# Optimization experiments

Measured on AMD Instinct MI355X. Metric: run time of the kernel, lower is better.

The kernel has to match this reference:

```python
import jax, jax.numpy as jnp
import numpy as np

X_SIZE, Y_SIZE, C_SIZE, H = 4, 2, 3, 128
B, C_CTX, T = 4, 512, 512


def _xavier(key, shape):
    fan_in, fan_out = shape[0], shape[1]
    a = jnp.sqrt(6.0 / (fan_in + fan_out))
    return jax.random.uniform(key, shape, jnp.float32, -a, a)


def setup_inputs() -> dict:
    key = jax.random.key(0)
    ks = jax.random.split(key, 9)
    return {
        "context_x": jax.random.normal(ks[0], (B, C_CTX, X_SIZE), jnp.float32),
        "context_y": jax.random.normal(ks[1], (B, C_CTX, Y_SIZE), jnp.float32),
        "target_x": jax.random.normal(ks[2], (B, T, X_SIZE), jnp.float32),
        "W_in": _xavier(ks[3], (C_SIZE + Y_SIZE, H)),
        "b_in": jnp.zeros((H,), jnp.float32),
        "W_ctx": _xavier(ks[4], (C_SIZE, H)),
        "b_ctx": jnp.zeros((H,), jnp.float32),
        "W_tgt": _xavier(ks[5], (H, H)),
        "b_tgt": jnp.zeros((H,), jnp.float32),
    }


def reference(context_x, context_y, target_x, W_in, b_in, W_ctx, b_ctx, W_tgt, b_tgt):
    ctx_c = context_x[..., :C_SIZE]                         # [B, C, c]
    # value: projected concat of context coords + context values
    enc_in = jnp.concatenate([ctx_c, context_y], axis=-1)   # [B, C, c+y]
    value = enc_in @ W_in + b_in                            # [B, C, H]
    key_ = ctx_c @ W_ctx + b_ctx                            # [B, C, H]
    query = target_x[..., :C_SIZE] @ W_ctx + b_ctx          # [B, T, H]
    # L1-distance attention scores: -sum_h |0.5*(key - query)|
    diff = (key_[:, None, :, :] - query[:, :, None, :]) * 0.5  # [B, T, C, H]
    scores = -jnp.sum(jnp.abs(diff), axis=-1)               # [B, T, C]
    w = jax.nn.softmax(scores, axis=-1)                     # [B, T, C]
    rep = jnp.einsum('btc,bch->bth', w, value)              # [B, T, H]
    return rep @ W_tgt + b_tgt
```

## Files before the change

kernel.cpp:

```cpp
#include <hip/hip_runtime.h>

#define BB 4
#define CC 512
#define TDIM 512
#define HH 128
#define TT 8
#define NR 4
#define CPW 128

__global__ __launch_bounds__(128) void prep_kernel(
    const float* __restrict__ ctx_x, const float* __restrict__ ctx_y,
    const float* __restrict__ tgt_x,
    const float* __restrict__ W_in, const float* __restrict__ b_in,
    const float* __restrict__ W_ctx, const float* __restrict__ b_ctx,
    float* __restrict__ key, float* __restrict__ query, float* __restrict__ value)
{
    int row = blockIdx.x;
    int h   = threadIdx.x;

    float4 cx = ((const float4*)ctx_x)[row];
    float2 cy = ((const float2*)ctx_y)[row];
    float4 tx = ((const float4*)tgt_x)[row];

    float wi0 = W_in[0*HH+h], wi1 = W_in[1*HH+h], wi2 = W_in[2*HH+h];
    float wi3 = W_in[3*HH+h], wi4 = W_in[4*HH+h];
    float wc0 = W_ctx[0*HH+h], wc1 = W_ctx[1*HH+h], wc2 = W_ctx[2*HH+h];
    float bi  = b_in[h], bc = b_ctx[h];

    value[row*HH+h] = fmaf(cx.x,wi0, fmaf(cx.y,wi1, fmaf(cx.z,wi2, fmaf(cy.x,wi3, fmaf(cy.y,wi4, bi)))));
    key  [row*HH+h] = fmaf(cx.x,wc0, fmaf(cx.y,wc1, fmaf(cx.z,wc2, bc)));
    query[row*HH+h] = fmaf(tx.x,wc0, fmaf(tx.y,wc1, fmaf(tx.z,wc2, bc)));
}

__global__ __launch_bounds__(512) void fused_kernel(
    const float* __restrict__ key, const float* __restrict__ query,
    const float* __restrict__ value, const float* __restrict__ W_tgt,
    const float* __restrict__ b_tgt, float* __restrict__ out)
{
    const int bx   = blockIdx.x;
    const int b    = bx >> 6;
    const int t0   = (bx & 63) * TT;
    const int tid  = threadIdx.x;
    const int wave = tid >> 6;
    const int cr   = wave & 3;
    const int th   = wave >> 2;
    const int lane = tid & 63;

    __shared__ __align__(16) float sbuf[8][4][128];
    __shared__ __align__(16) float pTbuf[8][128][4];
    __shared__ __align__(16) float2 ml[8][4];

    float (*rep)[HH]        = (float (*)[HH])&sbuf[0][0][0];
    float (*partial)[4][HH] = (float (*)[4][HH])&pTbuf[0][0][0];

    const int cl = lane >> 3;
    const int hq = lane & 7;
    float4 qr[4][4];
    #pragma unroll
    for (int tt = 0; tt < 4; ++tt)
        #pragma unroll
        for (int j = 0; j < 4; ++j)
            qr[tt][j] = *(const float4*)&query[(b*TDIM + t0 + th*4 + tt)*HH + j*32 + hq*4];

    #pragma unroll 1
    for (int pp = 0; pp < 4; ++pp) {
        const int crow = cr*CPW + pp*32 + cl*4;
        const float* kp = &key[(b*CC + crow)*HH];
        float a0[4], a1[4], a2[4], a3[4];
        #pragma unroll
        for (int tt = 0; tt < 4; ++tt) { a0[tt]=0.f; a1[tt]=0.f; a2[tt]=0.f; a3[tt]=0.f; }
        #pragma unroll
        for (int j = 0; j < 4; ++j) {
            const int hb = j*32 + hq*4;
            float4 k0 = *(const float4*)(kp + 0*HH + hb);
            float4 k1 = *(const float4*)(kp + 1*HH + hb);
            float4 k2 = *(const float4*)(kp + 2*HH + hb);
            float4 k3 = *(const float4*)(kp + 3*HH + hb);
            #pragma unroll
            for (int tt = 0; tt < 4; ++tt) {
                float4 qv = qr[tt][j];
                a0[tt] += fabsf(k0.x-qv.x)+fabsf(k0.y-qv.y)+fabsf(k0.z-qv.z)+fabsf(k0.w-qv.w);
                a1[tt] += fabsf(k1.x-qv.x)+fabsf(k1.y-qv.y)+fabsf(k1.z-qv.z)+fabsf(k1.w-qv.w);
                a2[tt] += fabsf(k2.x-qv.x)+fabsf(k2.y-qv.y)+fabsf(k2.z-qv.z)+fabsf(k2.w-qv.w);
                a3[tt] += fabsf(k3.x-qv.x)+fabsf(k3.y-qv.y)+fabsf(k3.z-qv.z)+fabsf(k3.w-qv.w);
            }
        }
        #pragma unroll
        for (int tt = 0; tt < 4; ++tt) {
            float v0=a0[tt], v1=a1[tt], v2=a2[tt], v3=a3[tt];
            v0 += __shfl_xor(v0,1); v0 += __shfl_xor(v0,2); v0 += __shfl_xor(v0,4);
            v1 += __shfl_xor(v1,1); v1 += __shfl_xor(v1,2); v1 += __shfl_xor(v1,4);
            v2 += __shfl_xor(v2,1); v2 += __shfl_xor(v2,2); v2 += __shfl_xor(v2,4);
            v3 += __shfl_xor(v3,1); v3 += __shfl_xor(v3,2); v3 += __shfl_xor(v3,4);
            if (hq == 0)
                *(float4*)&sbuf[wave][tt][pp*32 + cl*4] =
                    make_float4(-0.5f*v0, -0.5f*v1, -0.5f*v2, -0.5f*v3);
        }
    }

    {
        const int tg = lane >> 4, ci = lane & 15;
        float4 x0 = *(const float4*)&sbuf[wave][tg][ci*8];
        float4 x1 = *(const float4*)&sbuf[wave][tg][ci*8 + 4];
        float m = fmaxf(fmaxf(fmaxf(x0.x,x0.y), fmaxf(x0.z,x0.w)),
                        fmaxf(fmaxf(x1.x,x1.y), fmaxf(x1.z,x1.w)));
        m = fmaxf(m, __shfl_xor(m,1)); m = fmaxf(m, __shfl_xor(m,2));
        m = fmaxf(m, __shfl_xor(m,4)); m = fmaxf(m, __shfl_xor(m,8));
        float e0 = __expf(x0.x-m), e1 = __expf(x0.y-m), e2 = __expf(x0.z-m), e3 = __expf(x0.w-m);
        float e4 = __expf(x1.x-m), e5 = __expf(x1.y-m), e6 = __expf(x1.z-m), e7 = __expf(x1.w-m);
        float sm = ((e0+e1)+(e2+e3)) + ((e4+e5)+(e6+e7));
        sm += __shfl_xor(sm,1); sm += __shfl_xor(sm,2);
        sm += __shfl_xor(sm,4); sm += __shfl_xor(sm,8);
        pTbuf[wave][ci*8+0][tg] = e0;  pTbuf[wave][ci*8+1][tg] = e1;
        pTbuf[wave][ci*8+2][tg] = e2;  pTbuf[wave][ci*8+3][tg] = e3;
        pTbuf[wave][ci*8+4][tg] = e4;  pTbuf[wave][ci*8+5][tg] = e5;
        pTbuf[wave][ci*8+6][tg] = e6;  pTbuf[wave][ci*8+7][tg] = e7;
        if (ci == 0) ml[wave][tg] = make_float2(m, sm);
    }

    const int cs = lane >> 5, hv = lane & 31;
    {
        float4 acc[4];
        #pragma unroll
        for (int tt = 0; tt < 4; ++tt) acc[tt] = make_float4(0.f,0.f,0.f,0.f);
        const float* vp = &value[(b*CC + cr*CPW + cs*64)*HH + hv*4];
        #pragma unroll 4
        for (int i = 0; i < 64; ++i) {
            float4 p4 = *(const float4*)&pTbuf[wave][cs*64 + i][0];
            float4 vv = *(const float4*)(vp + i*HH);
            acc[0].x=fmaf(p4.x,vv.x,acc[0].x); acc[0].y=fmaf(p4.x,vv.y,acc[0].y);
            acc[0].z=fmaf(p4.x,vv.z,acc[0].z); acc[0].w=fmaf(p4.x,vv.w,acc[0].w);
            acc[1].x=fmaf(p4.y,vv.x,acc[1].x); acc[1].y=fmaf(p4.y,vv.y,acc[1].y);
            acc[1].z=fmaf(p4.y,vv.z,acc[1].z); acc[1].w=fmaf(p4.y,vv.w,acc[1].w);
            acc[2].x=fmaf(p4.z,vv.x,acc[2].x); acc[2].y=fmaf(p4.z,vv.y,acc[2].y);
            acc[2].z=fmaf(p4.z,vv.z,acc[2].z); acc[2].w=fmaf(p4.z,vv.w,acc[2].w);
            acc[3].x=fmaf(p4.w,vv.x,acc[3].x); acc[3].y=fmaf(p4.w,vv.y,acc[3].y);
            acc[3].z=fmaf(p4.w,vv.z,acc[3].z); acc[3].w=fmaf(p4.w,vv.w,acc[3].w);
        }
        #pragma unroll
        for (int tt = 0; tt < 4; ++tt) {
            acc[tt].x += __shfl_xor(acc[tt].x, 32);
            acc[tt].y += __shfl_xor(acc[tt].y, 32);
            acc[tt].z += __shfl_xor(acc[tt].z, 32);
            acc[tt].w += __shfl_xor(acc[tt].w, 32);
        }
        if (cs == 0) {
            #pragma unroll
            for (int tt = 0; tt < 4; ++tt)
                *(float4*)&partial[wave][tt][hv*4] = acc[tt];
        }
    }
    __syncthreads();

    #pragma unroll
    for (int e = tid; e < TT*HH; e += 512) {
        const int t = e >> 7, h = e & 127;
        const int thh = t >> 2, tt = t & 3;
        float2 q0 = ml[thh*4+0][tt], q1 = ml[thh*4+1][tt];
        float2 q2 = ml[thh*4+2][tt], q3 = ml[thh*4+3][tt];
        float M = fmaxf(fmaxf(q0.x,q1.x), fmaxf(q2.x,q3.x));
        float a0 = __expf(q0.x-M), a1 = __expf(q1.x-M);
        float a2 = __expf(q2.x-M), a3 = __expf(q3.x-M);
        float L = fmaf(a0,q0.y, fmaf(a1,q1.y, fmaf(a2,q2.y, a3*q3.y)));
        float r = a0*partial[thh*4+0][tt][h] + a1*partial[thh*4+1][tt][h]
                + a2*partial[thh*4+2][tt][h] + a3*partial[thh*4+3][tt][h];
        rep[t][h] = r / L;
    }
    __syncthreads();

    {
        const int lt = tid >> 7, h = tid & 127;
        float o0 = b_tgt[h], o1 = o0;
        for (int k = 0; k < HH; k += 4) {
            float4 r0 = *(const float4*)&rep[lt    ][k];
            float4 r1 = *(const float4*)&rep[lt + 4][k];
            float w0 = W_tgt[(k+0)*HH + h];
            float w1 = W_tgt[(k+1)*HH + h];
            float w2 = W_tgt[(k+2)*HH + h];
            float w3 = W_tgt[(k+3)*HH + h];
            o0 = fmaf(r0.x,w0, fmaf(r0.y,w1, fmaf(r0.z,w2, fmaf(r0.w,w3, o0))));
            o1 = fmaf(r1.x,w0, fmaf(r1.y,w1, fmaf(r1.z,w2, fmaf(r1.w,w3, o1))));
        }
        out[(b*TDIM + t0 + lt    )*HH + h] = o0;
        out[(b*TDIM + t0 + lt + 4)*HH + h] = o1;
    }
}

extern "C" void kernel_launch(void* const* d_in, const int* in_sizes, int n_in,
                              void* d_out, int out_size, void* d_ws, size_t ws_size,
                              hipStream_t stream) {
    const float* ctx_x = (const float*)d_in[0];
    const float* ctx_y = (const float*)d_in[1];
    const float* tgt_x = (const float*)d_in[2];
    const float* W_in  = (const float*)d_in[3];
    const float* b_in  = (const float*)d_in[4];
    const float* W_ctx = (const float*)d_in[5];
    const float* b_ctx = (const float*)d_in[6];
    const float* W_tgt = (const float*)d_in[7];
    const float* b_tgt = (const float*)d_in[8];

    float* ws    = (float*)d_ws;
    float* key   = ws;
    float* query = ws + 1*BB*CC*HH;
    float* value = ws + 2*BB*CC*HH;

    prep_kernel<<<BB*CC, 128, 0, stream>>>(ctx_x, ctx_y, tgt_x,
                                           W_in, b_in, W_ctx, b_ctx,
                                           key, query, value);
    fused_kernel<<<BB*(TDIM/TT), 512, 0, stream>>>(key, query, value,
                                                   W_tgt, b_tgt, (float*)d_out);
}
```

Before: 32.49 us.

## Split fused attention into context-split score/PV kernel plus separate projection kernel

Replaces the single fused kernel (256 blocks of 512 threads, 8 targets each) with a score+PV kernel over 1024 blocks of 256 threads, each handling 4 targets and half of the context. Partial softmax numerators and (max, sum) statistics go to workspace, and a new projection kernel merges the two halves and applies W_tgt. The goal is more blocks for better occupancy and load balance across the GPU. The cost is an extra kernel launch and a global-memory round trip for the partial results.

```diff
diff --git a/kernel.cpp b/kernel.cpp
--- a/kernel.cpp
+++ b/kernel.cpp
@@ -4,9 +4,6 @@
 #define CC 512
 #define TDIM 512
 #define HH 128
-#define TT 8
-#define NR 4
-#define CPW 128
 
 __global__ __launch_bounds__(128) void prep_kernel(
     const float* __restrict__ ctx_x, const float* __restrict__ ctx_y,
@@ -32,43 +29,43 @@
     query[row*HH+h] = fmaf(tx.x,wc0, fmaf(tx.y,wc1, fmaf(tx.z,wc2, bc)));
 }
 
-__global__ __launch_bounds__(512) void fused_kernel(
+__global__ __launch_bounds__(256) void score_pv_kernel(
     const float* __restrict__ key, const float* __restrict__ query,
-    const float* __restrict__ value, const float* __restrict__ W_tgt,
-    const float* __restrict__ b_tgt, float* __restrict__ out)
+    const float* __restrict__ value,
+    float* __restrict__ bp, float2* __restrict__ bml)
 {
-    const int bx   = blockIdx.x;
-    const int b    = bx >> 6;
-    const int t0   = (bx & 63) * TT;
-    const int tid  = threadIdx.x;
-    const int wave = tid >> 6;
-    const int cr   = wave & 3;
-    const int th   = wave >> 2;
-    const int lane = tid & 63;
-
-    __shared__ __align__(16) float sbuf[8][4][128];
-    __shared__ __align__(16) float pTbuf[8][128][4];
-    __shared__ __align__(16) float2 ml[8][4];
-
-    float (*rep)[HH]        = (float (*)[HH])&sbuf[0][0][0];
-    float (*partial)[4][HH] = (float (*)[4][HH])&pTbuf[0][0][0];
+    const int bx    = blockIdx.x;
+    const int chalf = bx & 1;
+    const int tq    = (bx >> 1) & 127;
+    const int b     = bx >> 8;
+    const int t0    = tq * 4;
+    const int c0    = chalf * 256;
+    const int tid   = threadIdx.x;
+    const int w     = tid >> 6;
+    const int lane  = tid & 63;
+
+    __shared__ __align__(16) float s_w[4][4][64];
+    __shared__ __align__(16) float pT_w[4][64][4];
+    __shared__ __align__(16) float2 wml[4][4];
+    __shared__ __align__(16) float partial[4][4][HH];
 
     const int cl = lane >> 3;
     const int hq = lane & 7;
     float4 qr[4][4];
     #pragma unroll
-    for (int tt = 0; tt < 4; ++tt)
+    for (int t = 0; t < 4; ++t)
         #pragma unroll
         for (int j = 0; j < 4; ++j)
-            qr[tt][j] = *(const float4*)&query[(b*TDIM + t0 + th*4 + tt)*HH + j*32 + hq*4];
+            qr[t][j] = *(const float4*)&query[(b*TDIM + t0 + t)*HH + j*32 + hq*4];
+
+    const int cw0 = c0 + w*64;
 
     #pragma unroll 1
-    for (int pp = 0; pp < 4; ++pp) {
-        const int crow = cr*CPW + pp*32 + cl*4;
-        const float* kp = &key[(b*CC + crow)*HH];
+    for (int pass = 0; pass < 2; ++pass) {
+        const float* kp = &key[(b*CC + cw0 + pass*32 + cl*4)*HH];
         float a0[4], a1[4], a2[4], a3[4];
         #pragma unroll
-        for (int tt = 0; tt < 4; ++tt) { a0[tt]=0.f; a1[tt]=0.f; a2[tt]=0.f; a3[tt]=0.f; }
+        for (int t = 0; t < 4; ++t) { a0[t]=0.f; a1[t]=0.f; a2[t]=0.f; a3[t]=0.f; }
         #pragma unroll
         for (int j = 0; j < 4; ++j) {
             const int hb = j*32 + hq*4;
@@ -77,56 +74,54 @@
             float4 k2 = *(const float4*)(kp + 2*HH + hb);
             float4 k3 = *(const float4*)(kp + 3*HH + hb);
             #pragma unroll
-            for (int tt = 0; tt < 4; ++tt) {
-                float4 qv = qr[tt][j];
-                a0[tt] += fabsf(k0.x-qv.x)+fabsf(k0.y-qv.y)+fabsf(k0.z-qv.z)+fabsf(k0.w-qv.w);
-                a1[tt] += fabsf(k1.x-qv.x)+fabsf(k1.y-qv.y)+fabsf(k1.z-qv.z)+fabsf(k1.w-qv.w);
-                a2[tt] += fabsf(k2.x-qv.x)+fabsf(k2.y-qv.y)+fabsf(k2.z-qv.z)+fabsf(k2.w-qv.w);
-                a3[tt] += fabsf(k3.x-qv.x)+fabsf(k3.y-qv.y)+fabsf(k3.z-qv.z)+fabsf(k3.w-qv.w);
+            for (int t = 0; t < 4; ++t) {
+                float4 qv = qr[t][j];
+                a0[t] += fabsf(k0.x-qv.x)+fabsf(k0.y-qv.y)+fabsf(k0.z-qv.z)+fabsf(k0.w-qv.w);
+                a1[t] += fabsf(k1.x-qv.x)+fabsf(k1.y-qv.y)+fabsf(k1.z-qv.z)+fabsf(k1.w-qv.w);
+                a2[t] += fabsf(k2.x-qv.x)+fabsf(k2.y-qv.y)+fabsf(k2.z-qv.z)+fabsf(k2.w-qv.w);
+                a3[t] += fabsf(k3.x-qv.x)+fabsf(k3.y-qv.y)+fabsf(k3.z-qv.z)+fabsf(k3.w-qv.w);
             }
         }
         #pragma unroll
-        for (int tt = 0; tt < 4; ++tt) {
-            float v0=a0[tt], v1=a1[tt], v2=a2[tt], v3=a3[tt];
+        for (int t = 0; t < 4; ++t) {
+            float v0=a0[t], v1=a1[t], v2=a2[t], v3=a3[t];
             v0 += __shfl_xor(v0,1); v0 += __shfl_xor(v0,2); v0 += __shfl_xor(v0,4);
             v1 += __shfl_xor(v1,1); v1 += __shfl_xor(v1,2); v1 += __shfl_xor(v1,4);
             v2 += __shfl_xor(v2,1); v2 += __shfl_xor(v2,2); v2 += __shfl_xor(v2,4);
             v3 += __shfl_xor(v3,1); v3 += __shfl_xor(v3,2); v3 += __shfl_xor(v3,4);
             if (hq == 0)
-                *(float4*)&sbuf[wave][tt][pp*32 + cl*4] =
+                *(float4*)&s_w[w][t][pass*32 + cl*4] =
                     make_float4(-0.5f*v0, -0.5f*v1, -0.5f*v2, -0.5f*v3);
         }
     }
 
     {
         const int tg = lane >> 4, ci = lane & 15;
-        float4 x0 = *(const float4*)&sbuf[wave][tg][ci*8];
-        float4 x1 = *(const float4*)&sbuf[wave][tg][ci*8 + 4];
-        float m = fmaxf(fmaxf(fmaxf(x0.x,x0.y), fmaxf(x0.z,x0.w)),
-                        fmaxf(fmaxf(x1.x,x1.y), fmaxf(x1.z,x1.w)));
+        float4 x = *(const float4*)&s_w[w][tg][ci*4];
+        float m = fmaxf(fmaxf(x.x, x.y), fmaxf(x.z, x.w));
         m = fmaxf(m, __shfl_xor(m,1)); m = fmaxf(m, __shfl_xor(m,2));
         m = fmaxf(m, __shfl_xor(m,4)); m = fmaxf(m, __shfl_xor(m,8));
-        float e0 = __expf(x0.x-m), e1 = __expf(x0.y-m), e2 = __expf(x0.z-m), e3 = __expf(x0.w-m);
-        float e4 = __expf(x1.x-m), e5 = __expf(x1.y-m), e6 = __expf(x1.z-m), e7 = __expf(x1.w-m);
-        float sm = ((e0+e1)+(e2+e3)) + ((e4+e5)+(e6+e7));
+        float e0 = __expf(x.x-m), e1 = __expf(x.y-m);
+        float e2 = __expf(x.z-m), e3 = __expf(x.w-m);
+        float sm = (e0+e1) + (e2+e3);
         sm += __shfl_xor(sm,1); sm += __shfl_xor(sm,2);
         sm += __shfl_xor(sm,4); sm += __shfl_xor(sm,8);
-        pTbuf[wave][ci*8+0][tg] = e0;  pTbuf[wave][ci*8+1][tg] = e1;
-        pTbuf[wave][ci*8+2][tg] = e2;  pTbuf[wave][ci*8+3][tg] = e3;
-        pTbuf[wave][ci*8+4][tg] = e4;  pTbuf[wave][ci*8+5][tg] = e5;
-        pTbuf[wave][ci*8+6][tg] = e6;  pTbuf[wave][ci*8+7][tg] = e7;
-        if (ci == 0) ml[wave][tg] = make_float2(m, sm);
-    }
-
-    const int cs = lane >> 5, hv = lane & 31;
+        pT_w[w][ci*4+0][tg] = e0;
+        pT_w[w][ci*4+1][tg] = e1;
+        pT_w[w][ci*4+2][tg] = e2;
+        pT_w[w][ci*4+3][tg] = e3;
+        if (ci == 0) wml[w][tg] = make_float2(m, sm);
+    }
+
     {
+        const int cs = lane >> 5, hv = lane & 31;
         float4 acc[4];
         #pragma unroll
-        for (int tt = 0; tt < 4; ++tt) acc[tt] = make_float4(0.f,0.f,0.f,0.f);
-        const float* vp = &value[(b*CC + cr*CPW + cs*64)*HH + hv*4];
-        #pragma unroll 4
-        for (int i = 0; i < 64; ++i) {
-            float4 p4 = *(const float4*)&pTbuf[wave][cs*64 + i][0];
+        for (int t = 0; t < 4; ++t) acc[t] = make_float4(0.f,0.f,0.f,0.f);
+        const float* vp = &value[(b*CC + cw0 + cs*32)*HH + hv*4];
+        #pragma unroll 8
+        for (int i = 0; i < 32; ++i) {
+            float4 p4 = *(const float4*)&pT_w[w][cs*32 + i][0];
             float4 vv = *(const float4*)(vp + i*HH);
             acc[0].x=fmaf(p4.x,vv.x,acc[0].x); acc[0].y=fmaf(p4.x,vv.y,acc[0].y);
             acc[0].z=fmaf(p4.x,vv.z,acc[0].z); acc[0].w=fmaf(p4.x,vv.w,acc[0].w);
@@ -138,33 +133,58 @@
             acc[3].z=fmaf(p4.w,vv.z,acc[3].z); acc[3].w=fmaf(p4.w,vv.w,acc[3].w);
         }
         #pragma unroll
-        for (int tt = 0; tt < 4; ++tt) {
-            acc[tt].x += __shfl_xor(acc[tt].x, 32);
-            acc[tt].y += __shfl_xor(acc[tt].y, 32);
-            acc[tt].z += __shfl_xor(acc[tt].z, 32);
-            acc[tt].w += __shfl_xor(acc[tt].w, 32);
+        for (int t = 0; t < 4; ++t) {
+            acc[t].x += __shfl_xor(acc[t].x, 32);
+            acc[t].y += __shfl_xor(acc[t].y, 32);
+            acc[t].z += __shfl_xor(acc[t].z, 32);
+            acc[t].w += __shfl_xor(acc[t].w, 32);
         }
         if (cs == 0) {
             #pragma unroll
-            for (int tt = 0; tt < 4; ++tt)
-                *(float4*)&partial[wave][tt][hv*4] = acc[tt];
+            for (int t = 0; t < 4; ++t)
+                *(float4*)&partial[w][t][hv*4] = acc[t];
         }
     }
     __syncthreads();
 
     #pragma unroll
-    for (int e = tid; e < TT*HH; e += 512) {
+    for (int e = tid; e < 4*HH; e += 256) {
         const int t = e >> 7, h = e & 127;
-        const int thh = t >> 2, tt = t & 3;
-        float2 q0 = ml[thh*4+0][tt], q1 = ml[thh*4+1][tt];
-        float2 q2 = ml[thh*4+2][tt], q3 = ml[thh*4+3][tt];
+        float2 q0 = wml[0][t], q1 = wml[1][t], q2 = wml[2][t], q3 = wml[3][t];
         float M = fmaxf(fmaxf(q0.x,q1.x), fmaxf(q2.x,q3.x));
         float a0 = __expf(q0.x-M), a1 = __expf(q1.x-M);
         float a2 = __expf(q2.x-M), a3 = __expf(q3.x-M);
-        float L = fmaf(a0,q0.y, fmaf(a1,q1.y, fmaf(a2,q2.y, a3*q3.y)));
-        float r = a0*partial[thh*4+0][tt][h] + a1*partial[thh*4+1][tt][h]
-                + a2*partial[thh*4+2][tt][h] + a3*partial[thh*4+3][tt][h];
-        rep[t][h] = r / L;
+        float r = a0*partial[0][t][h] + a1*partial[1][t][h]
+                + a2*partial[2][t][h] + a3*partial[3][t][h];
+        bp[bx*512 + e] = r;
+        if (h == 0) {
+            float L = fmaf(a0,q0.y, fmaf(a1,q1.y, fmaf(a2,q2.y, a3*q3.y)));
+            bml[bx*4 + t] = make_float2(M, L);
+        }
+    }
+}
+
+__global__ __launch_bounds__(256) void proj_kernel(
+    const float* __restrict__ bp, const float2* __restrict__ bml,
+    const float* __restrict__ W_tgt, const float* __restrict__ b_tgt,
+    float* __restrict__ out)
+{
+    const int bx  = blockIdx.x;
+    const int b   = bx >> 7;
+    const int t0  = (bx & 127) * 4;
+    const int tid = threadIdx.x;
+    const int blk0 = bx*2, blk1 = bx*2 + 1;
+
+    __shared__ __align__(16) float rep[4][HH];
+
+    #pragma unroll
+    for (int e = tid; e < 4*HH; e += 256) {
+        const int t = e >> 7;
+        float2 m0 = bml[blk0*4 + t], m1 = bml[blk1*4 + t];
+        float M  = fmaxf(m0.x, m1.x);
+        float a0 = __expf(m0.x - M), a1 = __expf(m1.x - M);
+        float invL = 1.f / fmaf(a0, m0.y, a1 * m1.y);
+        (&rep[0][0])[e] = (a0*bp[blk0*512 + e] + a1*bp[blk1*512 + e]) * invL;
     }
     __syncthreads();
 
@@ -173,7 +193,7 @@
         float o0 = b_tgt[h], o1 = o0;
         for (int k = 0; k < HH; k += 4) {
             float4 r0 = *(const float4*)&rep[lt    ][k];
-            float4 r1 = *(const float4*)&rep[lt + 4][k];
+            float4 r1 = *(const float4*)&rep[lt + 2][k];
             float w0 = W_tgt[(k+0)*HH + h];
             float w1 = W_tgt[(k+1)*HH + h];
             float w2 = W_tgt[(k+2)*HH + h];
@@ -182,7 +202,7 @@
             o1 = fmaf(r1.x,w0, fmaf(r1.y,w1, fmaf(r1.z,w2, fmaf(r1.w,w3, o1))));
         }
         out[(b*TDIM + t0 + lt    )*HH + h] = o0;
-        out[(b*TDIM + t0 + lt + 4)*HH + h] = o1;
+        out[(b*TDIM + t0 + lt + 2)*HH + h] = o1;
     }
 }
 
@@ -203,10 +223,12 @@
     float* key   = ws;
     float* query = ws + 1*BB*CC*HH;
     float* value = ws + 2*BB*CC*HH;
+    float* bp    = ws + 3*BB*CC*HH;
+    float2* bml  = (float2*)(bp + 1024*512);
 
     prep_kernel<<<BB*CC, 128, 0, stream>>>(ctx_x, ctx_y, tgt_x,
                                            W_in, b_in, W_ctx, b_ctx,
                                            key, query, value);
-    fused_kernel<<<BB*(TDIM/TT), 512, 0, stream>>>(key, query, value,
-                                                   W_tgt, b_tgt, (float*)d_out);
-}
+    score_pv_kernel<<<BB*128*2, 256, 0, stream>>>(key, query, value, bp, bml);
+    proj_kernel<<<BB*128, 256, 0, stream>>>(bp, bml, W_tgt, b_tgt, (float*)d_out);
+}
```

Result: slower. 38.55 us (+18.6%).

## Split context across eight waves per target group using 1024-thread blocks

Applied to the files above, without the earlier changes.

Doubles the block to 1024 threads so each group of four targets is handled by eight waves, each covering 64 context rows instead of 128. Partial softmax statistics and weighted sums are merged across eight waves in the combine step, and each thread then produces one output row. This roughly halves the serial per-wave work, adding latency hiding within the only 256 blocks. The cost is more shared memory, a wider merge and register pressure at 1024-thread launch bounds, which could limit occupancy.

```diff
diff --git a/kernel.cpp b/kernel.cpp
--- a/kernel.cpp
+++ b/kernel.cpp
@@ -5,8 +5,6 @@
 #define TDIM 512
 #define HH 128
 #define TT 8
-#define NR 4
-#define CPW 128
 
 __global__ __launch_bounds__(128) void prep_kernel(
     const float* __restrict__ ctx_x, const float* __restrict__ ctx_y,
@@ -32,7 +30,7 @@
     query[row*HH+h] = fmaf(tx.x,wc0, fmaf(tx.y,wc1, fmaf(tx.z,wc2, bc)));
 }
 
-__global__ __launch_bounds__(512) void fused_kernel(
+__global__ __launch_bounds__(1024) void fused_kernel(
     const float* __restrict__ key, const float* __restrict__ query,
     const float* __restrict__ value, const float* __restrict__ W_tgt,
     const float* __restrict__ b_tgt, float* __restrict__ out)
@@ -42,16 +40,15 @@
     const int t0   = (bx & 63) * TT;
     const int tid  = threadIdx.x;
     const int wave = tid >> 6;
-    const int cr   = wave & 3;
-    const int th   = wave >> 2;
+    const int th   = wave >> 3;
+    const int cw   = wave & 7;
     const int lane = tid & 63;
 
-    __shared__ __align__(16) float sbuf[8][4][128];
-    __shared__ __align__(16) float pTbuf[8][128][4];
-    __shared__ __align__(16) float2 ml[8][4];
-
-    float (*rep)[HH]        = (float (*)[HH])&sbuf[0][0][0];
-    float (*partial)[4][HH] = (float (*)[4][HH])&pTbuf[0][0][0];
+    __shared__ __align__(16) float s_w[16][4][64];
+    __shared__ __align__(16) float pT_w[16][64][4];
+    __shared__ __align__(16) float2 wml[16][4];
+    __shared__ __align__(16) float partial[16][4][HH];
+    __shared__ __align__(16) float rep[TT][HH];
 
     const int cl = lane >> 3;
     const int hq = lane & 7;
@@ -62,10 +59,11 @@
         for (int j = 0; j < 4; ++j)
             qr[tt][j] = *(const float4*)&query[(b*TDIM + t0 + th*4 + tt)*HH + j*32 + hq*4];
 
+    const int cw0 = cw * 64;
+
     #pragma unroll 1
-    for (int pp = 0; pp < 4; ++pp) {
-        const int crow = cr*CPW + pp*32 + cl*4;
-        const float* kp = &key[(b*CC + crow)*HH];
+    for (int pass = 0; pass < 2; ++pass) {
+        const float* kp = &key[(b*CC + cw0 + pass*32 + cl*4)*HH];
         float a0[4], a1[4], a2[4], a3[4];
         #pragma unroll
         for (int tt = 0; tt < 4; ++tt) { a0[tt]=0.f; a1[tt]=0.f; a2[tt]=0.f; a3[tt]=0.f; }
@@ -93,40 +91,38 @@
             v2 += __shfl_xor(v2,1); v2 += __shfl_xor(v2,2); v2 += __shfl_xor(v2,4);
             v3 += __shfl_xor(v3,1); v3 += __shfl_xor(v3,2); v3 += __shfl_xor(v3,4);
             if (hq == 0)
-                *(float4*)&sbuf[wave][tt][pp*32 + cl*4] =
+                *(float4*)&s_w[wave][tt][pass*32 + cl*4] =
                     make_float4(-0.5f*v0, -0.5f*v1, -0.5f*v2, -0.5f*v3);
         }
     }
 
     {
         const int tg = lane >> 4, ci = lane & 15;
-        float4 x0 = *(const float4*)&sbuf[wave][tg][ci*8];
-        float4 x1 = *(const float4*)&sbuf[wave][tg][ci*8 + 4];
-        float m = fmaxf(fmaxf(fmaxf(x0.x,x0.y), fmaxf(x0.z,x0.w)),
-                        fmaxf(fmaxf(x1.x,x1.y), fmaxf(x1.z,x1.w)));
+        float4 x = *(const float4*)&s_w[wave][tg][ci*4];
+        float m = fmaxf(fmaxf(x.x, x.y), fmaxf(x.z, x.w));
         m = fmaxf(m, __shfl_xor(m,1)); m = fmaxf(m, __shfl_xor(m,2));
         m = fmaxf(m, __shfl_xor(m,4)); m = fmaxf(m, __shfl_xor(m,8));
-        float e0 = __expf(x0.x-m), e1 = __expf(x0.y-m), e2 = __expf(x0.z-m), e3 = __expf(x0.w-m);
-        float e4 = __expf(x1.x-m), e5 = __expf(x1.y-m), e6 = __expf(x1.z-m), e7 = __expf(x1.w-m);
-        float sm = ((e0+e1)+(e2+e3)) + ((e4+e5)+(e6+e7));
+        float e0 = __expf(x.x-m), e1 = __expf(x.y-m);
+        float e2 = __expf(x.z-m), e3 = __expf(x.w-m);
+        float sm = (e0+e1) + (e2+e3);
         sm += __shfl_xor(sm,1); sm += __shfl_xor(sm,2);
         sm += __shfl_xor(sm,4); sm += __shfl_xor(sm,8);
-        pTbuf[wave][ci*8+0][tg] = e0;  pTbuf[wave][ci*8+1][tg] = e1;
-        pTbuf[wave][ci*8+2][tg] = e2;  pTbuf[wave][ci*8+3][tg] = e3;
-        pTbuf[wave][ci*8+4][tg] = e4;  pTbuf[wave][ci*8+5][tg] = e5;
-        pTbuf[wave][ci*8+6][tg] = e6;  pTbuf[wave][ci*8+7][tg] = e7;
-        if (ci == 0) ml[wave][tg] = make_float2(m, sm);
-    }
-
-    const int cs = lane >> 5, hv = lane & 31;
-    {
+        pT_w[wave][ci*4+0][tg] = e0;
+        pT_w[wave][ci*4+1][tg] = e1;
+        pT_w[wave][ci*4+2][tg] = e2;
+        pT_w[wave][ci*4+3][tg] = e3;
+        if (ci == 0) wml[wave][tg] = make_float2(m, sm);
+    }
+
+    {
+        const int cs = lane >> 5, hv = lane & 31;
         float4 acc[4];
         #pragma unroll
         for (int tt = 0; tt < 4; ++tt) acc[tt] = make_float4(0.f,0.f,0.f,0.f);
-        const float* vp = &value[(b*CC + cr*CPW + cs*64)*HH + hv*4];
-        #pragma unroll 4
-        for (int i = 0; i < 64; ++i) {
-            float4 p4 = *(const float4*)&pTbuf[wave][cs*64 + i][0];
+        const float* vp = &value[(b*CC + cw0 + cs*32)*HH + hv*4];
+        #pragma unroll 8
+        for (int i = 0; i < 32; ++i) {
+            float4 p4 = *(const float4*)&pT_w[wave][cs*32 + i][0];
             float4 vv = *(const float4*)(vp + i*HH);
             acc[0].x=fmaf(p4.x,vv.x,acc[0].x); acc[0].y=fmaf(p4.x,vv.y,acc[0].y);
             acc[0].z=fmaf(p4.x,vv.z,acc[0].z); acc[0].w=fmaf(p4.x,vv.w,acc[0].w);
@@ -152,37 +148,41 @@
     }
     __syncthreads();
 
-    #pragma unroll
-    for (int e = tid; e < TT*HH; e += 512) {
-        const int t = e >> 7, h = e & 127;
-        const int thh = t >> 2, tt = t & 3;
-        float2 q0 = ml[thh*4+0][tt], q1 = ml[thh*4+1][tt];
-        float2 q2 = ml[thh*4+2][tt], q3 = ml[thh*4+3][tt];
-        float M = fmaxf(fmaxf(q0.x,q1.x), fmaxf(q2.x,q3.x));
-        float a0 = __expf(q0.x-M), a1 = __expf(q1.x-M);
-        float a2 = __expf(q2.x-M), a3 = __expf(q3.x-M);
-        float L = fmaf(a0,q0.y, fmaf(a1,q1.y, fmaf(a2,q2.y, a3*q3.y)));
-        float r = a0*partial[thh*4+0][tt][h] + a1*partial[thh*4+1][tt][h]
-                + a2*partial[thh*4+2][tt][h] + a3*partial[thh*4+3][tt][h];
+    {
+        const int t = tid >> 7, h = tid & 127;
+        const int thh = t >> 2, tl = t & 3;
+        const int wbase = thh * 8;
+        float M = -1e30f;
+        float mj[8], lj[8];
+        #pragma unroll
+        for (int j = 0; j < 8; ++j) {
+            float2 q = wml[wbase + j][tl];
+            mj[j] = q.x; lj[j] = q.y;
+            M = fmaxf(M, q.x);
+        }
+        float L = 0.f, r = 0.f;
+        #pragma unroll
+        for (int j = 0; j < 8; ++j) {
+            float a = __expf(mj[j] - M);
+            L = fmaf(a, lj[j], L);
+            r = fmaf(a, partial[wbase + j][tl][h], r);
+        }
         rep[t][h] = r / L;
     }
     __syncthreads();
 
     {
         const int lt = tid >> 7, h = tid & 127;
-        float o0 = b_tgt[h], o1 = o0;
+        float o = b_tgt[h];
         for (int k = 0; k < HH; k += 4) {
-            float4 r0 = *(const float4*)&rep[lt    ][k];
-            float4 r1 = *(const float4*)&rep[lt + 4][k];
+            float4 r0 = *(const float4*)&rep[lt][k];
             float w0 = W_tgt[(k+0)*HH + h];
             float w1 = W_tgt[(k+1)*HH + h];
             float w2 = W_tgt[(k+2)*HH + h];
             float w3 = W_tgt[(k+3)*HH + h];
-            o0 = fmaf(r0.x,w0, fmaf(r0.y,w1, fmaf(r0.z,w2, fmaf(r0.w,w3, o0))));
-            o1 = fmaf(r1.x,w0, fmaf(r1.y,w1, fmaf(r1.z,w2, fmaf(r1.w,w3, o1))));
-        }
-        out[(b*TDIM + t0 + lt    )*HH + h] = o0;
-        out[(b*TDIM + t0 + lt + 4)*HH + h] = o1;
+            o = fmaf(r0.x,w0, fmaf(r0.y,w1, fmaf(r0.z,w2, fmaf(r0.w,w3, o))));
+        }
+        out[(b*TDIM + t0 + lt)*HH + h] = o;
     }
 }
 
@@ -207,6 +207,6 @@
     prep_kernel<<<BB*CC, 128, 0, stream>>>(ctx_x, ctx_y, tgt_x,
                                            W_in, b_in, W_ctx, b_ctx,
                                            key, query, value);
-    fused_kernel<<<BB*(TDIM/TT), 512, 0, stream>>>(key, query, value,
-                                                   W_tgt, b_tgt, (float*)d_out);
+    fused_kernel<<<BB*(TDIM/TT), 1024, 0, stream>>>(key, query, value,
+                                                    W_tgt, b_tgt, (float*)d_out);
 }
```

Measured after the change: 79.93 us. +146.0%, slower.
